# Kernel tuning notes

Measured on AMD Instinct MI355X. Metric: run time of the kernel, lower is better.

Reference implementation:

```python
import jax, jax.numpy as jnp
import numpy as np

B = 1024
NUM_DENSE = 13
NUM_SPARSE = 26
VOCAB = 100000
EMB_DIM = 16
BOT = [512, 256, 64, 16]
TOP = [1024, 512, 256]
D_INT = BOT[-1] + NUM_SPARSE * EMB_DIM  # 432
OUT_INT = D_INT * (D_INT + 1) // 2      # 93528


def setup_inputs() -> dict:
    key = jax.random.key(0)
    ks = jax.random.split(key, 32)
    inp = {
        "dense_features": jax.random.normal(ks[0], (B, NUM_DENSE), jnp.float32),
        "sparse_features": jax.random.randint(ks[1], (B, NUM_SPARSE), 0, VOCAB),
        "emb_tables": jax.random.normal(ks[2], (NUM_SPARSE, VOCAB, EMB_DIM), jnp.float32) * 0.02,
    }
    # bottom MLP weights (in, out) convention
    dims = [NUM_DENSE] + BOT
    for i in range(len(BOT)):
        inp[f"bw{i}"] = jax.random.normal(ks[3 + i], (dims[i], dims[i + 1]), jnp.float32) * 0.02
        inp[f"bb{i}"] = jnp.zeros((dims[i + 1],), jnp.float32)
    tdims = [BOT[-1] + OUT_INT] + TOP + [1]
    for i in range(len(TOP) + 1):
        inp[f"tw{i}"] = jax.random.normal(ks[10 + i], (tdims[i], tdims[i + 1]), jnp.float32) * 0.02
        inp[f"tb{i}"] = jnp.zeros((tdims[i + 1],), jnp.float32)
    return inp


def _forward(dense_features, emb_tables, bws, bbs, tws, tbs, sparse_features):
    # bottom MLP: Linear+ReLU stacks
    h = dense_features
    for w, b in zip(bws, bbs):
        h = jax.nn.relu(h @ w + b)
    dense_out = h  # (B, 16)
    # embedding lookups: table t indexed by column t of sparse_features
    # emb_tables: (F, V, E); gather per-table then flatten -> (B, F*E)
    emb = jnp.take_along_axis(
        emb_tables[None],  # (1, F, V, E)
        sparse_features.T[None, :, :, None].transpose(0, 1, 2, 3) * 0 + sparse_features.T[None, :, :, None],
        axis=2,
    )  # placeholder avoided below
    # cleaner: vmap over tables
    emb = jax.vmap(lambda tbl, idx: tbl[idx], in_axes=(0, 1))(emb_tables, sparse_features)  # (F, B, E)
    emb = jnp.transpose(emb, (1, 0, 2)).reshape(dense_features.shape[0], -1)  # (B, F*E)
    x = jnp.concatenate([dense_out, emb], axis=1)  # (B, D_INT)
    # pairwise interaction: upper triangle (incl. diagonal) of outer product.
    iu0, iu1 = np.triu_indices(x.shape[1])
    inter = x[:, iu0] * x[:, iu1]  # (B, OUT_INT) -- only needed entries
    z = jnp.concatenate([dense_out, inter], axis=1)
    n_top = len(tws)
    for i, (w, b) in enumerate(zip(tws, tbs)):
        z = z @ w + b
        if i < n_top - 1:
            z = jax.nn.relu(z)
    return z


def reference(dense_features, sparse_features, emb_tables,
              bw0, bb0, bw1, bb1, bw2, bb2, bw3, bb3,
              tw0, tb0, tw1, tb1, tw2, tb2, tw3, tb3):
    bws = [bw0, bw1, bw2, bw3]
    bbs = [bb0, bb1, bb2, bb3]
    tws = [tw0, tw1, tw2, tw3]
    tbs = [tb0, tb1, tb2, tb3]
    return _forward(dense_features, emb_tables, bws, bbs, tws, tbs, sparse_features)
```

## Files before the change

kernel.cpp:

```cpp
#include <hip/hip_runtime.h>
#include <stdint.h>

typedef unsigned short ushort_t;
typedef __attribute__((ext_vector_type(4))) float f32x4;
typedef __attribute__((ext_vector_type(8))) short s16x8;

#define DEVFN static __device__ __forceinline__

constexpr int B_   = 1024;
constexpr int P_   = 93528;
constexpr int K1   = 93544;
constexpr int Kp   = 94208;
constexpr int SPLITS = 16;
constexpr int KCH  = Kp / SPLITS;
constexpr int KSTEPS = KCH / 64;

DEVFN ushort_t f2bf(float f) {
  union { float f; unsigned int u; } x; x.f = f;
  unsigned int r = x.u + 0x7FFFu + ((x.u >> 16) & 1u);
  return (ushort_t)(r >> 16);
}

DEVFN void gload_lds16(const void* g, void* l) {
  __builtin_amdgcn_global_load_lds((const __attribute__((address_space(1))) unsigned int*)g,
                                   (__attribute__((address_space(3))) unsigned int*)l, 16, 0, 0);
}

__global__ __launch_bounds__(256) void k_pre(const float* __restrict__ dense,
    const int* __restrict__ sparse, const float* __restrict__ tbl,
    const float* __restrict__ bw0, const float* __restrict__ bb0,
    const float* __restrict__ bw1, const float* __restrict__ bb1,
    const float* __restrict__ bw2, const float* __restrict__ bb2,
    const float* __restrict__ bw3, const float* __restrict__ bb3,
    int* __restrict__ iu, float* __restrict__ xT) {
  __shared__ float sm[13520];
  int bid = blockIdx.x, t = threadIdx.x;
  if (bid < 368) {
    int k = bid * 256 + t;
    if (bid < 8) {
      int idx = bid * 256 + t;
      xT[432 * 1024 + idx] = (idx < 1024) ? 1.f : 0.f;
    }
    if (k >= Kp) return;
    int v;
    if (k < 16) v = k | (432 << 16);
    else if (k >= K1) v = 433 | (433 << 16);
    else {
      int p = k - 16;
      float s = sqrtf((float)(748225 - 8 * p));
      int i = (int)((865.0f - s) * 0.5f);
      if (i < 0) i = 0; if (i > 431) i = 431;
      while (i < 431 && (i + 1) * (865 - (i + 1)) / 2 <= p) ++i;
      while (i > 0 && i * (865 - i) / 2 > p) --i;
      int j = i + (p - i * (865 - i) / 2);
      v = i | (j << 16);
    }
    iu[k] = v;
  } else if (bid < 432) {
    float* xs = sm;
    float* h1 = sm + 208;
    float* h2 = h1 + 8192;
    float* h3 = h2 + 4096;
    int m0 = (bid - 368) * 16;
    if (t < 208) xs[t] = dense[m0 * 13 + t];
    __syncthreads();
    #pragma unroll
    for (int h = 0; h < 2; ++h) {
      int n = h * 256 + t;
      float a[16];
      float bv = bb0[n];
      #pragma unroll
      for (int r = 0; r < 16; ++r) a[r] = bv;
      for (int k = 0; k < 13; ++k) {
        float w = bw0[k * 512 + n];
        #pragma unroll
        for (int r = 0; r < 16; ++r) a[r] = fmaf(xs[r * 13 + k], w, a[r]);
      }
      #pragma unroll
      for (int r = 0; r < 16; ++r) h1[r * 512 + n] = fmaxf(a[r], 0.f);
    }
    __syncthreads();
    {
      int n = t;
      float a[16];
      float bv = bb1[n];
      #pragma unroll
      for (int r = 0; r < 16; ++r) a[r] = bv;
      for (int k = 0; k < 512; ++k) {
        float w = bw1[k * 256 + n];
        #pragma unroll
        for (int r = 0; r < 16; ++r) a[r] = fmaf(h1[r * 512 + k], w, a[r]);
      }
      #pragma unroll
      for (int r = 0; r < 16; ++r) h2[r * 256 + n] = fmaxf(a[r], 0.f);
    }
    __syncthreads();
    {
      int n = t & 63, r0 = t >> 6;
      float a[4];
      float bv = bb2[n];
      #pragma unroll
      for (int i = 0; i < 4; ++i) a[i] = bv;
      for (int k = 0; k < 256; ++k) {
        float w = bw2[k * 64 + n];
        #pragma unroll
        for (int i = 0; i < 4; ++i) a[i] = fmaf(h2[(r0 + 4 * i) * 256 + k], w, a[i]);
      }
      #pragma unroll
      for (int i = 0; i < 4; ++i) h3[(r0 + 4 * i) * 64 + n] = fmaxf(a[i], 0.f);
    }
    __syncthreads();
    {
      int n = t & 15, r = t >> 4;
      float a = bb3[n];
      for (int k = 0; k < 64; ++k) a = fmaf(h3[r * 64 + k], bw3[k * 16 + n], a);
      xT[(size_t)n * B_ + m0 + r] = fmaxf(a, 0.f);
    }
  } else {
    int e = bid - 432;
    int f = e >> 2;
    int b = (e & 3) * 256 + t;
    int idx = sparse[(size_t)b * 26 + f];
    const float4* src = (const float4*)(tbl + ((size_t)f * 100000 + idx) * 16);
    #pragma unroll
    for (int q = 0; q < 4; ++q) {
      float4 v = src[q];
      int r = 16 + f * 16 + q * 4;
      xT[(size_t)(r + 0) * B_ + b] = v.x;
      xT[(size_t)(r + 1) * B_ + b] = v.y;
      xT[(size_t)(r + 2) * B_ + b] = v.z;
      xT[(size_t)(r + 3) * B_ + b] = v.w;
    }
  }
}

__global__ __launch_bounds__(256, 8) void k_gz(const float* __restrict__ xT,
                                               const int* __restrict__ iu,
                                               const float* __restrict__ tw0,
                                               ushort_t* __restrict__ Z,
                                               ushort_t* __restrict__ WT) {
  __shared__ int ls_iu[512];
  int bid = blockIdx.x, t = threadIdx.x;
  int r3 = bid % 3;
  if (r3 == 0) {
    int idx = bid / 3;
    int l = t & 63, w = t >> 6;
    int mb = (idx & 15) * 64;
    int kt = (idx >> 4) * 512;
    ls_iu[t] = iu[kt + t];
    ls_iu[256 + t] = iu[kt + 256 + t];
    __syncthreads();
    uint32_t moff = mb + l;
    int kw = w * 128;
    #pragma unroll 2
    for (int g = 0; g < 16; ++g) {
      int kloc = kw + g * 8;
      int4 ij0 = *(const int4*)&ls_iu[kloc];
      int4 ij1 = *(const int4*)&ls_iu[kloc + 4];
      float p[8];
      {
        int v0 = ij0.x, v1 = ij0.y, v2 = ij0.z, v3 = ij0.w;
        p[0] = xT[(uint32_t)((v0 & 0xFFFF) << 10) + moff] * xT[(uint32_t)((v0 >> 16) << 10) + moff];
        p[1] = xT[(uint32_t)((v1 & 0xFFFF) << 10) + moff] * xT[(uint32_t)((v1 >> 16) << 10) + moff];
        p[2] = xT[(uint32_t)((v2 & 0xFFFF) << 10) + moff] * xT[(uint32_t)((v2 >> 16) << 10) + moff];
        p[3] = xT[(uint32_t)((v3 & 0xFFFF) << 10) + moff] * xT[(uint32_t)((v3 >> 16) << 10) + moff];
        v0 = ij1.x; v1 = ij1.y; v2 = ij1.z; v3 = ij1.w;
        p[4] = xT[(uint32_t)((v0 & 0xFFFF) << 10) + moff] * xT[(uint32_t)((v0 >> 16) << 10) + moff];
        p[5] = xT[(uint32_t)((v1 & 0xFFFF) << 10) + moff] * xT[(uint32_t)((v1 >> 16) << 10) + moff];
        p[6] = xT[(uint32_t)((v2 & 0xFFFF) << 10) + moff] * xT[(uint32_t)((v2 >> 16) << 10) + moff];
        p[7] = xT[(uint32_t)((v3 & 0xFFFF) << 10) + moff] * xT[(uint32_t)((v3 >> 16) << 10) + moff];
      }
      union { uint32_t w4[4]; int4 v4; } o;
      asm("v_cvt_pk_bf16_f32 %0, %1, %2" : "=v"(o.w4[0]) : "v"(p[0]), "v"(p[1]));
      asm("v_cvt_pk_bf16_f32 %0, %1, %2" : "=v"(o.w4[1]) : "v"(p[2]), "v"(p[3]));
      asm("v_cvt_pk_bf16_f32 %0, %1, %2" : "=v"(o.w4[2]) : "v"(p[4]), "v"(p[5]));
      asm("v_cvt_pk_bf16_f32 %0, %1, %2" : "=v"(o.w4[3]) : "v"(p[6]), "v"(p[7]));
      int kglob = kt + kloc;
      *(int4*)&Z[((size_t)(kglob >> 3) * 1024 + moff) * 8] = o.v4;
    }
  } else {
    int idx = (bid / 3) * 2 + r3 - 1;
    int k0 = (idx % 368) * 256, n0 = (idx / 368) * 64;
    int nl = t & 63, kq = t >> 6;
    int n = n0 + nl;
    int kbase = k0 + kq * 64;
    const float* src = tw0 + (size_t)kbase * 1024 + n;
    ushort_t* dst = WT + ((size_t)(kbase >> 3) * 1024 + n) * 8;
    bool full = (kbase + 64 <= K1);
    #pragma unroll
    for (int g = 0; g < 8; ++g) {
      float v[8];
      if (full) {
        #pragma unroll
        for (int e = 0; e < 8; ++e) v[e] = src[(size_t)(g * 8 + e) << 10];
      } else {
        #pragma unroll
        for (int e = 0; e < 8; ++e) {
          int k = kbase + g * 8 + e;
          v[e] = (k < K1) ? src[(size_t)(g * 8 + e) << 10] : 0.f;
        }
      }
      union { uint32_t w4[4]; int4 v4; } o;
      asm("v_cvt_pk_bf16_f32 %0, %1, %2" : "=v"(o.w4[0]) : "v"(v[0]), "v"(v[1]));
      asm("v_cvt_pk_bf16_f32 %0, %1, %2" : "=v"(o.w4[1]) : "v"(v[2]), "v"(v[3]));
      asm("v_cvt_pk_bf16_f32 %0, %1, %2" : "=v"(o.w4[2]) : "v"(v[4]), "v"(v[5]));
      asm("v_cvt_pk_bf16_f32 %0, %1, %2" : "=v"(o.w4[3]) : "v"(v[6]), "v"(v[7]));
      *(int4*)(dst + (size_t)g * 8192) = o.v4;
    }
  }
}

__global__ __launch_bounds__(512, 2) void k_gemm(const ushort_t* __restrict__ Z,
                                                 const ushort_t* __restrict__ WT,
                                                 float* __restrict__ part) {
  __shared__ ushort_t lds[65536];
  int t = threadIdx.x;
  int bid = blockIdx.x;
  int x = bid & 7, r = bid >> 3;
  int g = (x << 3) | (r & 7);
  int s = g >> 2;
  int m0 = (g & 3) * 256, n0 = (r >> 3) * 256;
  int kb = s * KCH;

  int rr = t >> 3, cc = t & 7;
  int cs = cc ^ (rr & 7);
  const ushort_t* pa0 = Z  + (((size_t)(kb >> 3) + cs) * 1024 + m0 + rr) * 8;
  const ushort_t* pb0 = WT + (((size_t)(kb >> 3) + cs) * 1024 + n0 + rr) * 8;
  int l0 = t * 8;

  int w = t >> 6, l = t & 63;
  int wm = (w >> 2) * 128, wn = (w & 3) * 64;
  int lhi = l >> 4, llo = l & 15;

  f32x4 acc[8][4];
  #pragma unroll
  for (int a = 0; a < 8; ++a)
    #pragma unroll
    for (int b = 0; b < 4; ++b) acc[a][b] = f32x4{0.f, 0.f, 0.f, 0.f};

  #pragma unroll
  for (int i = 0; i < 4; ++i)
    gload_lds16(pb0 + i * 512, &lds[32768 + i * 4096 + l0]);
  gload_lds16(pa0,           &lds[0 * 4096 + l0]);
  gload_lds16(pa0 + 2 * 512, &lds[2 * 4096 + l0]);
  gload_lds16(pa0 + 1 * 512, &lds[1 * 4096 + l0]);
  gload_lds16(pa0 + 3 * 512, &lds[3 * 4096 + l0]);
  #pragma unroll
  for (int i = 0; i < 4; ++i)
    gload_lds16(pb0 + 65536 + i * 512, &lds[32768 + 16384 + i * 4096 + l0]);

  for (int tt = 0; tt < KSTEPS; ++tt) {
    const ushort_t* Ab = &lds[(tt & 1) * 16384];
    const ushort_t* Bb = &lds[32768 + (tt & 1) * 16384];
    bool pf  = (tt + 1 < KSTEPS);
    bool pf2 = (tt + 2 < KSTEPS);
    ushort_t* dA  = &lds[((tt + 1) & 1) * 16384];
    ushort_t* dB2 = &lds[32768 + (tt & 1) * 16384];
    const ushort_t* sA  = pa0 + (size_t)(tt + 1) * 65536;
    const ushort_t* sB2 = pb0 + (size_t)(tt + 2) * 65536;
    s16x8 bf[4][2];

    if (pf) asm volatile("s_waitcnt vmcnt(6)" ::: "memory");
    else    asm volatile("s_waitcnt vmcnt(2)" ::: "memory");
    asm volatile("s_waitcnt lgkmcnt(0)" ::: "memory");
    __builtin_amdgcn_s_barrier();
    if (pf) {
      gload_lds16(sA,           dA + l0);
      gload_lds16(sA + 2 * 512, dA + 2 * 4096 + l0);
    }
    #pragma unroll
    for (int nf = 0; nf < 4; ++nf)
      #pragma unroll
      for (int ks = 0; ks < 2; ++ks) {
        int row = wn + nf * 16 + llo;
        int ch = (ks * 4 + lhi) ^ (row & 7);
        bf[nf][ks] = *(const s16x8*)&Bb[row * 64 + ch * 8];
      }
    #pragma unroll
    for (int q = 0; q < 4; ++q) {
      if (q == 1 && pf) {
        gload_lds16(sA + 1 * 512, dA + 1 * 4096 + l0);
        gload_lds16(sA + 3 * 512, dA + 3 * 4096 + l0);
      }
      if (q == 2) {
        if (pf) asm volatile("s_waitcnt vmcnt(8)" ::: "memory");
        else    asm volatile("s_waitcnt vmcnt(0)" ::: "memory");
        asm volatile("s_waitcnt lgkmcnt(0)" ::: "memory");
        __builtin_amdgcn_s_barrier();
        if (pf2) {
          #pragma unroll
          for (int i = 0; i < 4; ++i)
            gload_lds16(sB2 + i * 512, dB2 + i * 4096 + l0);
        }
      }
      s16x8 af[2][2];
      #pragma unroll
      for (int j = 0; j < 2; ++j)
        #pragma unroll
        for (int ks = 0; ks < 2; ++ks) {
          int row = wm + (q * 2 + j) * 16 + llo;
          int ch = (ks * 4 + lhi) ^ (row & 7);
          af[j][ks] = *(const s16x8*)&Ab[row * 64 + ch * 8];
        }
      #pragma unroll
      for (int j = 0; j < 2; ++j)
        #pragma unroll
        for (int nf = 0; nf < 4; ++nf)
          #pragma unroll
          for (int ks = 0; ks < 2; ++ks)
            acc[q * 2 + j][nf] = __builtin_amdgcn_mfma_f32_16x16x32_bf16(af[j][ks], bf[nf][ks], acc[q * 2 + j][nf], 0, 0, 0);
    }
  }

  float* pbase = part + ((size_t)s << 20);
  #pragma unroll
  for (int mf = 0; mf < 8; ++mf)
    #pragma unroll
    for (int nf = 0; nf < 4; ++nf) {
      int n = n0 + wn + nf * 16 + llo;
      #pragma unroll
      for (int r2 = 0; r2 < 4; ++r2) {
        int m = m0 + wm + mf * 16 + lhi * 4 + r2;
        pbase[(size_t)m * 1024 + n] = acc[mf][nf][r2];
      }
    }
}

__global__ __launch_bounds__(256) void k_red(const float* __restrict__ part,
                                             const float* __restrict__ bias,
                                             float* __restrict__ z1) {
  int idx = blockIdx.x * 256 + threadIdx.x;
  float a = bias[idx & 1023];
  #pragma unroll
  for (int s = 0; s < SPLITS; ++s) a += part[((size_t)s << 20) + idx];
  z1[idx] = fmaxf(a, 0.f);
}

template<int K, int N>
__global__ __launch_bounds__(256) void k_sgemm(const float* __restrict__ A,
                                               const float* __restrict__ W,
                                               const float* __restrict__ bias,
                                               float* __restrict__ C) {
  __shared__ float As[16][34];
  __shared__ float Bs[16][68];
  int t = threadIdx.x;
  int m0 = blockIdx.x * 32, n0 = blockIdx.y * 64;
  int tx = t & 15, ty = t >> 4;
  float acc[2][4];
  #pragma unroll
  for (int j = 0; j < 2; ++j)
    #pragma unroll
    for (int q = 0; q < 4; ++q) acc[j][q] = 0.f;
  int ar = t >> 3, ak = (t & 7) * 2;
  int bk = t >> 4, bn = (t & 15) * 4;
  for (int k0 = 0; k0 < K; k0 += 16) {
    float2 av = *(const float2*)&A[(size_t)(m0 + ar) * K + k0 + ak];
    float4 bv = *(const float4*)&W[(size_t)(k0 + bk) * N + n0 + bn];
    __syncthreads();
    As[ak][ar] = av.x; As[ak + 1][ar] = av.y;
    *(float4*)&Bs[bk][bn] = bv;
    __syncthreads();
    #pragma unroll
    for (int k = 0; k < 16; ++k) {
      float2 a = *(const float2*)&As[k][ty * 2];
      float4 b = *(const float4*)&Bs[k][tx * 4];
      acc[0][0] = fmaf(a.x, b.x, acc[0][0]); acc[0][1] = fmaf(a.x, b.y, acc[0][1]);
      acc[0][2] = fmaf(a.x, b.z, acc[0][2]); acc[0][3] = fmaf(a.x, b.w, acc[0][3]);
      acc[1][0] = fmaf(a.y, b.x, acc[1][0]); acc[1][1] = fmaf(a.y, b.y, acc[1][1]);
      acc[1][2] = fmaf(a.y, b.z, acc[1][2]); acc[1][3] = fmaf(a.y, b.w, acc[1][3]);
    }
  }
  #pragma unroll
  for (int j = 0; j < 2; ++j) {
    int m = m0 + ty * 2 + j;
    float4 o;
    o.x = fmaxf(acc[j][0] + bias[n0 + tx * 4 + 0], 0.f);
    o.y = fmaxf(acc[j][1] + bias[n0 + tx * 4 + 1], 0.f);
    o.z = fmaxf(acc[j][2] + bias[n0 + tx * 4 + 2], 0.f);
    o.w = fmaxf(acc[j][3] + bias[n0 + tx * 4 + 3], 0.f);
    *(float4*)&C[(size_t)m * N + n0 + tx * 4] = o;
  }
}

__global__ __launch_bounds__(256) void k_last(const float* __restrict__ z3,
                                              const float* __restrict__ w,
                                              const float* __restrict__ bias,
                                              float* __restrict__ out) {
  int t = threadIdx.x, l = t & 63, wv = t >> 6;
  int m = blockIdx.x * 4 + wv;
  float s = 0.f;
  #pragma unroll
  for (int c = 0; c < 4; ++c) s = fmaf(z3[(size_t)m * 256 + c * 64 + l], w[c * 64 + l], s);
  #pragma unroll
  for (int off = 32; off; off >>= 1) s += __shfl_down(s, off, 64);
  if (l == 0) out[m] = s + bias[0];
}

__global__ __launch_bounds__(256) void k_z1init(const float* __restrict__ bias, float* __restrict__ z1) {
  int idx = blockIdx.x * 256 + threadIdx.x;
  z1[idx] = bias[idx & 1023];
}
__global__ __launch_bounds__(256) void k_relu(float* __restrict__ z1) {
  int idx = blockIdx.x * 256 + threadIdx.x;
  z1[idx] = fmaxf(z1[idx], 0.f);
}
constexpr int FB_S = 8;
__global__ __launch_bounds__(256) void k_fbgemm(const float* __restrict__ xT,
                                                const int* __restrict__ iu,
                                                const float* __restrict__ tw0,
                                                float* __restrict__ z1) {
  __shared__ float zs[32 * 64];
  __shared__ float wsb[32 * 64];
  int t = threadIdx.x;
  int m0 = blockIdx.x * 64, n0 = blockIdx.y * 64, s = blockIdx.z;
  int kch = (K1 + FB_S - 1) / FB_S;
  int k0 = s * kch, kend = min(k0 + kch, K1);
  float acc[16];
  #pragma unroll
  for (int q = 0; q < 16; ++q) acc[q] = 0.f;
  int mm = t & 63, ng = t >> 6;
  for (int kk = k0; kk < kend; kk += 32) {
    __syncthreads();
    for (int sl = t; sl < 2048; sl += 256) {
      int kloc = sl >> 6, v6 = sl & 63;
      int k = kk + kloc;
      float zv = 0.f, wv = 0.f;
      if (k < kend) {
        int ij = iu[k];
        int i = ij & 0xFFFF, j = ij >> 16;
        zv = xT[(size_t)i * B_ + m0 + v6] * xT[(size_t)j * B_ + m0 + v6];
        wv = tw0[(size_t)k * 1024 + n0 + v6];
      }
      zs[kloc * 64 + v6] = zv;
      wsb[kloc * 64 + v6] = wv;
    }
    __syncthreads();
    #pragma unroll 4
    for (int kloc = 0; kloc < 32; ++kloc) {
      float zv = zs[kloc * 64 + mm];
      #pragma unroll
      for (int q = 0; q < 16; ++q)
        acc[q] = fmaf(zv, wsb[kloc * 64 + ng * 16 + q], acc[q]);
    }
  }
  #pragma unroll
  for (int q = 0; q < 16; ++q)
    atomicAdd(&z1[(size_t)(m0 + mm) * 1024 + n0 + ng * 16 + q], acc[q]);
}

extern "C" void kernel_launch(void* const* d_in, const int* in_sizes, int n_in,
                              void* d_out, int out_size, void* d_ws, size_t ws_size,
                              hipStream_t stream) {
  const float* dense  = (const float*)d_in[0];
  const int*   sparse = (const int*)  d_in[1];
  const float* emb    = (const float*)d_in[2];
  const float* bw0 = (const float*)d_in[3];  const float* bb0 = (const float*)d_in[4];
  const float* bw1 = (const float*)d_in[5];  const float* bb1 = (const float*)d_in[6];
  const float* bw2 = (const float*)d_in[7];  const float* bb2 = (const float*)d_in[8];
  const float* bw3 = (const float*)d_in[9];  const float* bb3 = (const float*)d_in[10];
  const float* tw0 = (const float*)d_in[11]; const float* tb0 = (const float*)d_in[12];
  const float* tw1 = (const float*)d_in[13]; const float* tb1 = (const float*)d_in[14];
  const float* tw2 = (const float*)d_in[15]; const float* tb2 = (const float*)d_in[16];
  const float* tw3 = (const float*)d_in[17]; const float* tb3 = (const float*)d_in[18];
  float* out = (float*)d_out;

  char* ws = (char*)d_ws;
  size_t off = 0;
  auto alloc = [&](size_t bytes) -> char* {
    char* p = ws + off;
    off = (off + bytes + 255) & ~(size_t)255;
    return p;
  };
  float* xT = (float*)alloc((size_t)434 * 1024 * 4);
  int*   iu = (int*)  alloc((size_t)Kp * 4);
  float* z1 = (float*)alloc((size_t)1024 * 1024 * 4);
  float* z2 = (float*)alloc((size_t)1024 * 512 * 4);
  float* z3 = (float*)alloc((size_t)1024 * 256 * 4);
  ushort_t* Z    = (ushort_t*)alloc((size_t)1024 * Kp * 2);
  ushort_t* WT   = (ushort_t*)alloc((size_t)1024 * Kp * 2);
  float*    part = (float*)   alloc((size_t)SPLITS * 1024 * 1024 * 4);
  bool big = (off <= ws_size);

  k_pre<<<536, 256, 0, stream>>>(dense, sparse, emb, bw0, bb0, bw1, bb1, bw2, bb2, bw3, bb3, iu, xT);

  if (big) {
    k_gz<<<8832, 256, 0, stream>>>(xT, iu, tw0, Z, WT);
    k_gemm<<<256, 512, 0, stream>>>(Z, WT, part);
    k_red<<<4096, 256, 0, stream>>>(part, tb0, z1);
  } else {
    k_z1init<<<4096, 256, 0, stream>>>(tb0, z1);
    k_fbgemm<<<dim3(16, 16, FB_S), 256, 0, stream>>>(xT, iu, tw0, z1);
    k_relu<<<4096, 256, 0, stream>>>(z1);
  }

  k_sgemm<1024, 512><<<dim3(32, 8), 256, 0, stream>>>(z1, tw1, tb1, z2);
  k_sgemm<512, 256><<<dim3(32, 4), 256, 0, stream>>>(z2, tw2, tb2, z3);
  k_last<<<256, 256, 0, stream>>>(z3, tw3, tb3, out);
}
```

Before: 547.8 us.

## Restructure split-K GEMM loop into four ping-pong phases with prioritized MFMA

The split-K bf16 GEMM main loop is rewritten as four phases per K-step. A fragments are double-buffered in registers (afX/afY), so LDS reads for the next phase are issued before the current phase's MFMAs. Global-to-LDS prefetches of A and B are spread across the phases, and each MFMA block is wrapped in barriers, sched_barrier and s_setprio. The aim is to hide LDS and global latency behind matrix work. In exchange the loop has more barriers per step and more register pressure. The next step's A fragment is read right after a per-thread vmcnt wait with no workgroup barrier first, which risks reading LDS that other threads have not finished filling.

```diff
diff --git a/kernel.cpp b/kernel.cpp
--- a/kernel.cpp
+++ b/kernel.cpp
@@ -238,79 +238,101 @@
     #pragma unroll
     for (int b = 0; b < 4; ++b) acc[a][b] = f32x4{0.f, 0.f, 0.f, 0.f};
 
-  #pragma unroll
-  for (int i = 0; i < 4; ++i)
-    gload_lds16(pb0 + i * 512, &lds[32768 + i * 4096 + l0]);
-  gload_lds16(pa0,           &lds[0 * 4096 + l0]);
-  gload_lds16(pa0 + 2 * 512, &lds[2 * 4096 + l0]);
-  gload_lds16(pa0 + 1 * 512, &lds[1 * 4096 + l0]);
-  gload_lds16(pa0 + 3 * 512, &lds[3 * 4096 + l0]);
-  #pragma unroll
-  for (int i = 0; i < 4; ++i)
-    gload_lds16(pb0 + 65536 + i * 512, &lds[32768 + 16384 + i * 4096 + l0]);
+  s16x8 bf[4][2], afX[4], afY[4];
+
+  auto rdA = [&](s16x8* dst, int mfb, const ushort_t* Ab) {
+    #pragma unroll
+    for (int j = 0; j < 2; ++j)
+      #pragma unroll
+      for (int ks = 0; ks < 2; ++ks) {
+        int row = wm + (mfb + j) * 16 + llo;
+        int ch = (ks * 4 + lhi) ^ (row & 7);
+        dst[j * 2 + ks] = *(const s16x8*)&Ab[row * 64 + ch * 8];
+      }
+  };
+  auto rdB = [&](const ushort_t* Bb) {
+    #pragma unroll
+    for (int nf = 0; nf < 4; ++nf)
+      #pragma unroll
+      for (int ks = 0; ks < 2; ++ks) {
+        int row = wn + nf * 16 + llo;
+        int ch = (ks * 4 + lhi) ^ (row & 7);
+        bf[nf][ks] = *(const s16x8*)&Bb[row * 64 + ch * 8];
+      }
+  };
+
+#define MFMA_PHASE(P, AF)                                                        \
+  __builtin_amdgcn_s_barrier();                                                  \
+  asm volatile("s_waitcnt lgkmcnt(0)" ::: "memory");                             \
+  __builtin_amdgcn_sched_barrier(0);                                             \
+  __builtin_amdgcn_s_setprio(1);                                                 \
+  _Pragma("unroll")                                                              \
+  for (int j = 0; j < 2; ++j)                                                    \
+    _Pragma("unroll")                                                            \
+    for (int nf = 0; nf < 4; ++nf)                                               \
+      _Pragma("unroll")                                                          \
+      for (int ks = 0; ks < 2; ++ks)                                             \
+        acc[(P) * 2 + j][nf] = __builtin_amdgcn_mfma_f32_16x16x32_bf16(          \
+            AF[j * 2 + ks], bf[nf][ks], acc[(P) * 2 + j][nf], 0, 0, 0);          \
+  __builtin_amdgcn_s_setprio(0);                                                 \
+  __builtin_amdgcn_sched_barrier(0);                                             \
+  __builtin_amdgcn_s_barrier();
+
+  #pragma unroll
+  for (int i = 0; i < 4; ++i) gload_lds16(pa0 + i * 512, &lds[i * 4096 + l0]);
+  #pragma unroll
+  for (int i = 0; i < 4; ++i) gload_lds16(pb0 + i * 512, &lds[32768 + i * 4096 + l0]);
+  #pragma unroll
+  for (int i = 0; i < 4; ++i) gload_lds16(pb0 + 65536 + i * 512, &lds[32768 + 16384 + i * 4096 + l0]);
+  asm volatile("s_waitcnt vmcnt(4)" ::: "memory");
+  __builtin_amdgcn_s_barrier();
+  rdA(afX, 0, &lds[0]);
 
   for (int tt = 0; tt < KSTEPS; ++tt) {
     const ushort_t* Ab = &lds[(tt & 1) * 16384];
+    const ushort_t* An = &lds[((tt + 1) & 1) * 16384];
     const ushort_t* Bb = &lds[32768 + (tt & 1) * 16384];
-    bool pf  = (tt + 1 < KSTEPS);
-    bool pf2 = (tt + 2 < KSTEPS);
     ushort_t* dA  = &lds[((tt + 1) & 1) * 16384];
     ushort_t* dB2 = &lds[32768 + (tt & 1) * 16384];
     const ushort_t* sA  = pa0 + (size_t)(tt + 1) * 65536;
     const ushort_t* sB2 = pb0 + (size_t)(tt + 2) * 65536;
-    s16x8 bf[4][2];
-
-    if (pf) asm volatile("s_waitcnt vmcnt(6)" ::: "memory");
-    else    asm volatile("s_waitcnt vmcnt(2)" ::: "memory");
-    asm volatile("s_waitcnt lgkmcnt(0)" ::: "memory");
-    __builtin_amdgcn_s_barrier();
-    if (pf) {
-      gload_lds16(sA,           dA + l0);
-      gload_lds16(sA + 2 * 512, dA + 2 * 4096 + l0);
-    }
-    #pragma unroll
-    for (int nf = 0; nf < 4; ++nf)
-      #pragma unroll
-      for (int ks = 0; ks < 2; ++ks) {
-        int row = wn + nf * 16 + llo;
-        int ch = (ks * 4 + lhi) ^ (row & 7);
-        bf[nf][ks] = *(const s16x8*)&Bb[row * 64 + ch * 8];
-      }
-    #pragma unroll
-    for (int q = 0; q < 4; ++q) {
-      if (q == 1 && pf) {
-        gload_lds16(sA + 1 * 512, dA + 1 * 4096 + l0);
-        gload_lds16(sA + 3 * 512, dA + 3 * 4096 + l0);
-      }
-      if (q == 2) {
-        if (pf) asm volatile("s_waitcnt vmcnt(8)" ::: "memory");
-        else    asm volatile("s_waitcnt vmcnt(0)" ::: "memory");
-        asm volatile("s_waitcnt lgkmcnt(0)" ::: "memory");
-        __builtin_amdgcn_s_barrier();
-        if (pf2) {
-          #pragma unroll
-          for (int i = 0; i < 4; ++i)
-            gload_lds16(sB2 + i * 512, dB2 + i * 4096 + l0);
-        }
-      }
-      s16x8 af[2][2];
-      #pragma unroll
-      for (int j = 0; j < 2; ++j)
-        #pragma unroll
-        for (int ks = 0; ks < 2; ++ks) {
-          int row = wm + (q * 2 + j) * 16 + llo;
-          int ch = (ks * 4 + lhi) ^ (row & 7);
-          af[j][ks] = *(const s16x8*)&Ab[row * 64 + ch * 8];
-        }
-      #pragma unroll
-      for (int j = 0; j < 2; ++j)
-        #pragma unroll
-        for (int nf = 0; nf < 4; ++nf)
-          #pragma unroll
-          for (int ks = 0; ks < 2; ++ks)
-            acc[q * 2 + j][nf] = __builtin_amdgcn_mfma_f32_16x16x32_bf16(af[j][ks], bf[nf][ks], acc[q * 2 + j][nf], 0, 0, 0);
-    }
-  }
+    bool pf1 = (tt + 1 < KSTEPS);
+    bool pf2 = (tt + 2 < KSTEPS);
+
+    rdB(Bb);
+    rdA(afY, 2, Ab);
+    if (pf1) {
+      gload_lds16(sA,       dA + l0);
+      gload_lds16(sA + 512, dA + 4096 + l0);
+    }
+    MFMA_PHASE(0, afX)
+
+    rdA(afX, 4, Ab);
+    if (pf1) {
+      gload_lds16(sA + 1024, dA + 2 * 4096 + l0);
+      gload_lds16(sA + 1536, dA + 3 * 4096 + l0);
+    }
+    MFMA_PHASE(1, afY)
+
+    rdA(afY, 6, Ab);
+    if (pf2) {
+      gload_lds16(sB2,       dB2 + l0);
+      gload_lds16(sB2 + 512, dB2 + 4096 + l0);
+    }
+    MFMA_PHASE(2, afX)
+
+    if (pf1) {
+      if (pf2) asm volatile("s_waitcnt vmcnt(2)" ::: "memory");
+      else     asm volatile("s_waitcnt vmcnt(0)" ::: "memory");
+      rdA(afX, 0, An);
+    }
+    if (pf2) {
+      gload_lds16(sB2 + 1024, dB2 + 2 * 4096 + l0);
+      gload_lds16(sB2 + 1536, dB2 + 3 * 4096 + l0);
+    }
+    MFMA_PHASE(3, afY)
+  }
+#undef MFMA_PHASE
 
   float* pbase = part + ((size_t)s << 20);
   #pragma unroll
```

After: 530.3 us. -3.2%, faster.
